# Kernel optimization log

Hardware: AMD Instinct MI355X
Metric: run time of the kernel (lower is better)

The kernel has to match this reference:

```python
import jax, jax.numpy as jnp
import numpy as np

B, N, D, C = 32, 6, 41, 64
FH, FW = 4, 6            # 150//32, 200//32
IN_CH = 768
NX, NY, NZ = 200, 200, 1 # from x/y/zbound
DX = np.array([0.5, 0.5, 20.0], np.float32)
BX = np.array([-49.75, -49.75, 0.0], np.float32)  # bound[0] + step/2


def _frustum():
    # (D, FH, FW, 3) pixel-coord + depth frustum, matching create_frustum
    ds = np.arange(4.0, 45.0, 1.0, dtype=np.float32)             # D = 41
    xs = np.linspace(0.0, 200.0 - 1.0, FW, dtype=np.float32)
    ys = np.linspace(0.0, 150.0 - 1.0, FH, dtype=np.float32)
    g = np.stack(np.broadcast_arrays(xs[None, None, :], ys[None, :, None], ds[:, None, None]), axis=-1)
    return jnp.asarray(g)


def setup_inputs() -> dict:
    key = jax.random.key(0)
    k1, k2, k3 = jax.random.split(key, 3)
    x = jax.random.normal(k1, (B, N, IN_CH, FH, FW), jnp.float32)
    # cam-to-ego base rotation (cam z -> ego x, cam x -> -ego y, cam y -> -ego z)
    R0 = np.array([[0., 0., 1.], [-1., 0., 0.], [0., -1., 0.]], np.float32)
    yaw = 2.0 * np.pi * np.arange(N) / N
    cz, sz = np.cos(yaw).astype(np.float32), np.sin(yaw).astype(np.float32)
    Rz = np.zeros((N, 3, 3), np.float32)
    Rz[:, 0, 0] = cz; Rz[:, 0, 1] = -sz; Rz[:, 1, 0] = sz; Rz[:, 1, 1] = cz; Rz[:, 2, 2] = 1.0
    rots = jnp.asarray(np.broadcast_to((Rz @ R0)[None], (B, N, 3, 3)))
    K = np.array([[100., 0., 100.], [0., 100., 75.], [0., 0., 1.]], np.float32)
    intrins = jnp.asarray(np.broadcast_to(K, (B, N, 3, 3)))
    trans = jax.random.uniform(k2, (B, N, 3), jnp.float32, -2.0, 2.0)
    conv_w = jax.random.normal(k3, (D + C, IN_CH), jnp.float32) * 0.02
    conv_b = jnp.zeros((D + C,), jnp.float32)
    return {"x": x, "rots": rots, "trans": trans, "intrins": intrins, "conv_w": conv_w, "conv_b": conv_b}


def reference(x, rots, trans, intrins, conv_w, conv_b):
    frustum = _frustum()                                        # (D,FH,FW,3)
    # --- get_geometry ---
    pts = jnp.concatenate([frustum[..., :2] * frustum[..., 2:3], frustum[..., 2:3]], -1)
    combine = rots @ jnp.linalg.inv(intrins)                    # (B,N,3,3)
    geom = jnp.einsum('bnij,dhwj->bndhwi', combine, pts) + trans[:, :, None, None, None, :]
    # --- get_cam_feats: 1x1 conv depthnet, softmax depth, outer product ---
    xf = x.reshape(B * N, IN_CH, FH, FW)
    y = jnp.einsum('oc,bchw->bohw', conv_w, xf) + conv_b[None, :, None, None]
    depth_logit = y[:, :D]                                      # (BN,D,FH,FW)
    depth = jax.nn.softmax(depth_logit, axis=1)
    feat = y[:, D:D + C]                                        # (BN,C,FH,FW)
    xv = (depth[:, None] * feat[:, :, None]).reshape(B, N, C, D, FH, FW).transpose(0, 1, 3, 4, 5, 2)
    # --- voxel_pooling: segment-sum over voxel rank, scatter to BEV ---
    xN = xv.reshape(-1, C)                                      # (Nprime, C)
    g = ((geom - (BX - DX / 2.0)) / DX).astype(jnp.int32).reshape(-1, 3)  # trunc like .long()
    Np = xN.shape[0]
    bix = jnp.repeat(jnp.arange(Np // (Np // B) * 0 + B), Np // B)        # batch index per point
    kept = ((g[:, 0] >= 0) & (g[:, 0] < NX) & (g[:, 1] >= 0) & (g[:, 1] < NY)
            & (g[:, 2] >= 0) & (g[:, 2] < NZ))
    idx = ((bix * NZ + g[:, 2]) * NX + g[:, 0]) * NY + g[:, 1]
    idx = jnp.where(kept, idx, 0)
    xm = jnp.where(kept[:, None], xN, 0.0)
    pooled = jax.ops.segment_sum(xm, idx, num_segments=B * NZ * NX * NY)  # (B*NZ*NX*NY, C)
    final = pooled.reshape(B, NZ, NX, NY, C).transpose(0, 1, 4, 2, 3).reshape(B, NZ * C, NX, NY)
    return (final, depth_logit)
```

## Files before the change

kernel.cpp:

```cpp
#include <hip/hip_runtime.h>
#include <hip/hip_bf16.h>

#define B_    32
#define N_    6
#define D_    41
#define C_    64
#define FH_   4
#define FW_   6
#define INCH  768
#define HW    24
#define O_    105
#define PBN   984
#define PPB   5904
#define NPTS  188928
#define FINAL_ELEMS 81920000


__global__ __launch_bounds__(256) void k_conv(
    const float* __restrict__ x, const float* __restrict__ w,
    const float* __restrict__ bias,
    float* __restrict__ depth_ws, float* __restrict__ feat_ws,
    float* __restrict__ dlogit)
{
    const int bn = blockIdx.x;
    const int t  = threadIdx.x;
    __shared__ float ylds[O_ * HW];
    __shared__ float smax[HW], srs[HW];

    const float* xb0 = x + (size_t)bn * (INCH * HW);
    for (int u2 = t; u2 < O_ * 6; u2 += 256) {
        int o  = u2 / 6;
        int hq = (u2 % 6) * 4;
        const float* wr = w + (size_t)o * INCH;
        const float* xb = xb0 + hq;
        float a0 = 0.f, a1 = 0.f, a2 = 0.f, a3 = 0.f;
        for (int c = 0; c < INCH; ++c) {
            float wv = wr[c];
            float4 xv = *(const float4*)(xb + c * HW);
            a0 = __fadd_rn(a0, __fmul_rn(wv, xv.x));
            a1 = __fadd_rn(a1, __fmul_rn(wv, xv.y));
            a2 = __fadd_rn(a2, __fmul_rn(wv, xv.z));
            a3 = __fadd_rn(a3, __fmul_rn(wv, xv.w));
        }
        float bo = bias[o];
        ylds[o * HW + hq + 0] = __fadd_rn(a0, bo);
        ylds[o * HW + hq + 1] = __fadd_rn(a1, bo);
        ylds[o * HW + hq + 2] = __fadd_rn(a2, bo);
        ylds[o * HW + hq + 3] = __fadd_rn(a3, bo);
    }
    __syncthreads();

    if (t < HW) {
        float mx = -1e30f;
        for (int d = 0; d < D_; d++) mx = fmaxf(mx, ylds[d * HW + t]);
        float s = 0.f;
        for (int d = 0; d < D_; d++) s = __fadd_rn(s, expf(__fsub_rn(ylds[d * HW + t], mx)));
        smax[t] = mx; srs[t] = s;
    }
    __syncthreads();

    for (int u = t; u < D_ * HW; u += 256) {
        float yv = ylds[u];
        int hw = u % HW;
        depth_ws[bn * PBN + u] = __fdiv_rn(expf(__fsub_rn(yv, smax[hw])), srs[hw]);
        dlogit[(size_t)bn * PBN + u] = yv;
    }
    for (int u = t; u < C_ * HW; u += 256)
        feat_ws[bn * (C_ * HW) + u] = ylds[D_ * HW + u];
}

__global__ __launch_bounds__(256) void k_geom(
    const float* __restrict__ m1, const float* __restrict__ trans,
    const float* __restrict__ m2, int* __restrict__ vox)
{
    const float* rots = (fabsf(m1[0]) > 50.0f) ? m2 : m1;
    const float* intr = (fabsf(m1[0]) > 50.0f) ? m1 : m2;

    int p = blockIdx.x * 256 + threadIdx.x;
    int b  = p / PPB;
    int pl = p % PPB;
    int n  = pl / PBN;
    int r  = pl % PBN;
    int d  = r / HW;
    int hw = r % HW;
    int h = hw / FW_, wp = hw % FW_;

    float dv = 4.0f + (float)d;
    float xi = (float)((double)wp * (199.0 / 5.0));
    float yi = (float)((double)h  * (149.0 / 3.0));
    float px = __fmul_rn(xi, dv), py = __fmul_rn(yi, dv), pz = dv;

    int bn = b * N_ + n;
    const float* K = intr + bn * 9;
    const float* R = rots + bn * 9;
    const float* T = trans + bn * 3;

    float a00 = K[0], a01 = K[1], a02 = K[2];
    float a11 = K[4], a12 = K[5];
    float a22 = K[8];

    float i00 = __fdiv_rn(1.0f, a00);
    float i11 = __fdiv_rn(1.0f, a11);
    float x0  = __fmul_rn(a01, i00);
    float i01 = __fmul_rn(-i11, x0);
    float i22 = __fdiv_rn(1.0f, a22);
    float y0  = __fmul_rn(a02, i00);
    y0 = __fadd_rn(y0, __fmul_rn(a12, i01));
    float y1  = __fmul_rn(a12, i11);
    float i02 = __fmul_rn(-i22, y0);
    float i12 = __fmul_rn(-i22, y1);
    float i10 = 0.f, i20 = 0.f, i21 = 0.f;

    float r00 = R[0], r01 = R[1], r02 = R[2];
    float r10 = R[3], r11 = R[4], r12 = R[5];
    float r20 = R[6], r21 = R[7], r22 = R[8];

#define MM(u0,u1,u2, v0,v1,v2) \
    __fmaf_rn(u2, v2, __fmaf_rn(u1, v1, __fmul_rn(u0, v0)))
    float c00 = MM(r00, r01, r02, i00, i10, i20);
    float c01 = MM(r00, r01, r02, i01, i11, i21);
    float c02 = MM(r00, r01, r02, i02, i12, i22);
    float c10 = MM(r10, r11, r12, i00, i10, i20);
    float c11 = MM(r10, r11, r12, i01, i11, i21);
    float c12 = MM(r10, r11, r12, i02, i12, i22);
    float c20 = MM(r20, r21, r22, i00, i10, i20);
    float c21 = MM(r20, r21, r22, i01, i11, i21);
    float c22 = MM(r20, r21, r22, i02, i12, i22);
#undef MM

#define DOT3(u0,v0,u1,v1,u2,v2) \
    __fadd_rn(__fadd_rn(__fmul_rn(u0,v0), __fmul_rn(u1,v1)), __fmul_rn(u2,v2))
    float gx = __fadd_rn(DOT3(c00,px, c01,py, c02,pz), T[0]);
    float gy = __fadd_rn(DOT3(c10,px, c11,py, c12,pz), T[1]);
    float gz = __fadd_rn(DOT3(c20,px, c21,py, c22,pz), T[2]);
#undef DOT3

    int ix = (int)__fmul_rn(__fadd_rn(gx, 50.0f), 2.0f);
    int iy = (int)__fmul_rn(__fadd_rn(gy, 50.0f), 2.0f);
    int iz = (int)__fdiv_rn(__fadd_rn(gz, 10.0f), 20.0f);
    bool kept = (ix >= 0) && (ix < 200) && (iy >= 0) && (iy < 200) && (iz == 0);
    vox[p] = kept ? (ix * 200 + iy) : -1;
}

__global__ __launch_bounds__(256) void k_splat(
    const float* __restrict__ depth, const float* __restrict__ feat,
    const int* __restrict__ vox, float* __restrict__ out)
{
    __shared__ float plane[10000];
    int bid = blockIdx.x;
    int b   = bid >> 8;
    int rem = bid & 255;
    int c   = rem >> 2;
    int q   = rem & 3;
    int t   = threadIdx.x;

    for (int i = t; i < 10000; i += 256) plane[i] = 0.f;
    __syncthreads();

    const int lo = q * 10000;
    const float* fb = feat + (size_t)(b * N_) * (C_ * HW) + c * HW;
    for (int i = t; i < PPB; i += 256) {
        int p = b * PPB + i;
        int rel = vox[p] - lo;
        if ((unsigned)rel < 10000u) {
            int n  = i / PBN;
            int hw = i % HW;
            atomicAdd(&plane[rel], depth[p] * fb[n * (C_ * HW) + hw]);
        }
    }
    __syncthreads();

    float4* ob = (float4*)(out + ((size_t)(b * C_ + c) * 40000) + lo);
    const float4* pl4 = (const float4*)plane;
    for (int i = t; i < 2500; i += 256) ob[i] = pl4[i];
}

extern "C" void kernel_launch(void* const* d_in, const int* in_sizes, int n_in,
                              void* d_out, int out_size, void* d_ws, size_t ws_size,
                              hipStream_t stream) {
    const float *x = nullptr, *m1 = nullptr, *m2 = nullptr, *trn = nullptr,
                *w = nullptr, *bias = nullptr;
    for (int i = 0; i < n_in; i++) {
        const float* p = (const float*)d_in[i];
        switch (in_sizes[i]) {
            case 3538944: x = p; break;
            case 1728:    if (!m1) m1 = p; else m2 = p; break;
            case 576:     trn = p; break;
            case 80640:   w = p; break;
            case 105:     bias = p; break;
            default: break;
        }
    }
    if (!x)    x    = (const float*)d_in[0];
    if (!m1)   m1   = (const float*)d_in[1];
    if (!trn)  trn  = (const float*)d_in[2];
    if (!m2)   m2   = (const float*)d_in[3];
    if (!w)    w    = (const float*)d_in[4];
    if (!bias) bias = (const float*)d_in[5];

    float* depth_ws = (float*)d_ws;
    float* feat_ws  = depth_ws + NPTS;
    int*   vox      = (int*)(feat_ws + 192 * C_ * HW);

    float* out    = (float*)d_out;
    float* dlogit = out + FINAL_ELEMS;

    k_conv <<<192,  256, 0, stream>>>(x, w, bias, depth_ws, feat_ws, dlogit);
    k_geom <<<738,  256, 0, stream>>>(m1, trn, m2, vox);
    k_splat<<<8192, 256, 0, stream>>>(depth_ws, feat_ws, vox, out);
}
```

Before: 537.8 us.

## Split conv into a 576-block kernel and a separate softmax kernel

The 1x1 conv is split out of the fused conv+softmax kernel. Each camera's 630 output work items are now spread over 3 blocks of 210 threads, so 576 blocks run instead of 192, and the raw logits go to a global workspace. A separate softmax kernel reads that workspace to write depth probabilities and logits, and the splat kernel reads feature channels straight from the workspace, which drops the separate feature copy. This is meant to fill more of the GPU's compute units during the conv, at the cost of one extra launch and a round trip of the logits through global memory.

New measurement: 520.1 us. 3.3% less time.

```diff
diff --git a/kernel.cpp b/kernel.cpp
--- a/kernel.cpp
+++ b/kernel.cpp
@@ -13,60 +13,66 @@
 #define PBN   984
 #define PPB   5904
 #define NPTS  188928
+#define YSTR  2520
 #define FINAL_ELEMS 81920000
 
 
-__global__ __launch_bounds__(256) void k_conv(
+__global__ __launch_bounds__(256) void k_conv_y(
     const float* __restrict__ x, const float* __restrict__ w,
-    const float* __restrict__ bias,
-    float* __restrict__ depth_ws, float* __restrict__ feat_ws,
-    float* __restrict__ dlogit)
+    const float* __restrict__ bias, float* __restrict__ y_ws)
+{
+    const int bid  = blockIdx.x;
+    const int bn   = bid / 3;
+    const int part = bid % 3;
+    const int t    = threadIdx.x;
+    if (t >= 210) return;
+    const int u2 = part * 210 + t;
+    const int o  = u2 / 6;
+    const int hq = (u2 % 6) * 4;
+
+    const float* wr = w + (size_t)o * INCH;
+    const float* xb = x + (size_t)bn * (INCH * HW) + hq;
+    float a0 = 0.f, a1 = 0.f, a2 = 0.f, a3 = 0.f;
+    for (int c = 0; c < INCH; ++c) {
+        float wv = wr[c];
+        float4 xv = *(const float4*)(xb + c * HW);
+        a0 = __fadd_rn(a0, __fmul_rn(wv, xv.x));
+        a1 = __fadd_rn(a1, __fmul_rn(wv, xv.y));
+        a2 = __fadd_rn(a2, __fmul_rn(wv, xv.z));
+        a3 = __fadd_rn(a3, __fmul_rn(wv, xv.w));
+    }
+    float bo = bias[o];
+    float* dst = y_ws + (size_t)bn * YSTR + o * HW + hq;
+    dst[0] = __fadd_rn(a0, bo);
+    dst[1] = __fadd_rn(a1, bo);
+    dst[2] = __fadd_rn(a2, bo);
+    dst[3] = __fadd_rn(a3, bo);
+}
+
+__global__ __launch_bounds__(256) void k_softmax(
+    const float* __restrict__ y_ws,
+    float* __restrict__ depth_ws, float* __restrict__ dlogit)
 {
     const int bn = blockIdx.x;
     const int t  = threadIdx.x;
-    __shared__ float ylds[O_ * HW];
     __shared__ float smax[HW], srs[HW];
-
-    const float* xb0 = x + (size_t)bn * (INCH * HW);
-    for (int u2 = t; u2 < O_ * 6; u2 += 256) {
-        int o  = u2 / 6;
-        int hq = (u2 % 6) * 4;
-        const float* wr = w + (size_t)o * INCH;
-        const float* xb = xb0 + hq;
-        float a0 = 0.f, a1 = 0.f, a2 = 0.f, a3 = 0.f;
-        for (int c = 0; c < INCH; ++c) {
-            float wv = wr[c];
-            float4 xv = *(const float4*)(xb + c * HW);
-            a0 = __fadd_rn(a0, __fmul_rn(wv, xv.x));
-            a1 = __fadd_rn(a1, __fmul_rn(wv, xv.y));
-            a2 = __fadd_rn(a2, __fmul_rn(wv, xv.z));
-            a3 = __fadd_rn(a3, __fmul_rn(wv, xv.w));
-        }
-        float bo = bias[o];
-        ylds[o * HW + hq + 0] = __fadd_rn(a0, bo);
-        ylds[o * HW + hq + 1] = __fadd_rn(a1, bo);
-        ylds[o * HW + hq + 2] = __fadd_rn(a2, bo);
-        ylds[o * HW + hq + 3] = __fadd_rn(a3, bo);
-    }
-    __syncthreads();
+    const float* yb = y_ws + (size_t)bn * YSTR;
 
     if (t < HW) {
         float mx = -1e30f;
-        for (int d = 0; d < D_; d++) mx = fmaxf(mx, ylds[d * HW + t]);
+        for (int d = 0; d < D_; d++) mx = fmaxf(mx, yb[d * HW + t]);
         float s = 0.f;
-        for (int d = 0; d < D_; d++) s = __fadd_rn(s, expf(__fsub_rn(ylds[d * HW + t], mx)));
+        for (int d = 0; d < D_; d++) s = __fadd_rn(s, expf(__fsub_rn(yb[d * HW + t], mx)));
         smax[t] = mx; srs[t] = s;
     }
     __syncthreads();
 
     for (int u = t; u < D_ * HW; u += 256) {
-        float yv = ylds[u];
+        float yv = yb[u];
         int hw = u % HW;
         depth_ws[bn * PBN + u] = __fdiv_rn(expf(__fsub_rn(yv, smax[hw])), srs[hw]);
         dlogit[(size_t)bn * PBN + u] = yv;
     }
-    for (int u = t; u < C_ * HW; u += 256)
-        feat_ws[bn * (C_ * HW) + u] = ylds[D_ * HW + u];
 }
 
 __global__ __launch_bounds__(256) void k_geom(
@@ -143,7 +149,7 @@
 }
 
 __global__ __launch_bounds__(256) void k_splat(
-    const float* __restrict__ depth, const float* __restrict__ feat,
+    const float* __restrict__ depth, const float* __restrict__ y_ws,
     const int* __restrict__ vox, float* __restrict__ out)
 {
     __shared__ float plane[10000];
@@ -158,14 +164,14 @@
     __syncthreads();
 
     const int lo = q * 10000;
-    const float* fb = feat + (size_t)(b * N_) * (C_ * HW) + c * HW;
+    const float* fb = y_ws + (size_t)(b * N_) * YSTR + (D_ + c) * HW;
     for (int i = t; i < PPB; i += 256) {
         int p = b * PPB + i;
         int rel = vox[p] - lo;
         if ((unsigned)rel < 10000u) {
             int n  = i / PBN;
             int hw = i % HW;
-            atomicAdd(&plane[rel], depth[p] * fb[n * (C_ * HW) + hw]);
+            atomicAdd(&plane[rel], depth[p] * fb[n * YSTR + hw]);
         }
     }
     __syncthreads();
@@ -198,14 +204,15 @@
     if (!w)    w    = (const float*)d_in[4];
     if (!bias) bias = (const float*)d_in[5];
 
-    float* depth_ws = (float*)d_ws;
-    float* feat_ws  = depth_ws + NPTS;
-    int*   vox      = (int*)(feat_ws + 192 * C_ * HW);
+    float* y_ws     = (float*)d_ws;
+    float* depth_ws = y_ws + 192 * YSTR;
+    int*   vox      = (int*)(depth_ws + NPTS);
 
     float* out    = (float*)d_out;
     float* dlogit = out + FINAL_ELEMS;
 
-    k_conv <<<192,  256, 0, stream>>>(x, w, bias, depth_ws, feat_ws, dlogit);
-    k_geom <<<738,  256, 0, stream>>>(m1, trn, m2, vox);
-    k_splat<<<8192, 256, 0, stream>>>(depth_ws, feat_ws, vox, out);
-}
+    k_conv_y <<<576,  256, 0, stream>>>(x, w, bias, y_ws);
+    k_softmax<<<192,  256, 0, stream>>>(y_ws, depth_ws, dlogit);
+    k_geom   <<<738,  256, 0, stream>>>(m1, trn, m2, vox);
+    k_splat  <<<8192, 256, 0, stream>>>(depth_ws, y_ws, vox, out);
+}
```

## Stage input tile in LDS and register-block conv over 3 outputs

Applied to the files above, without the earlier changes.

The 1x1 conv kernel now loads each camera's input slice into shared memory in two halves. Each thread computes 3 output channels by 4 pixels with float4 weight loads and fma, so every x value read is reused across three outputs instead of being refetched from global memory per output. This is meant to cut global load traffic and instruction count in the conv, which was the serial per-block dot-product bottleneck. Using fma instead of separate rounded mul and add changes rounding slightly, and the workspace buffers are reordered.

New measurement: 458.5 us. -14.7%, faster.

```diff
diff --git a/kernel.cpp b/kernel.cpp
--- a/kernel.cpp
+++ b/kernel.cpp
@@ -16,57 +16,101 @@
 #define FINAL_ELEMS 81920000
 
 
-__global__ __launch_bounds__(256) void k_conv(
+__global__ __launch_bounds__(256) void k_conv_fused(
     const float* __restrict__ x, const float* __restrict__ w,
     const float* __restrict__ bias,
-    float* __restrict__ depth_ws, float* __restrict__ feat_ws,
+    float* __restrict__ feat_ws, float* __restrict__ depth_ws,
     float* __restrict__ dlogit)
 {
+    __shared__ float xs[9216];
+    __shared__ float ys[O_ * HW];
+    __shared__ float smax[HW], srs[HW];
+
     const int bn = blockIdx.x;
     const int t  = threadIdx.x;
-    __shared__ float ylds[O_ * HW];
-    __shared__ float smax[HW], srs[HW];
-
-    const float* xb0 = x + (size_t)bn * (INCH * HW);
-    for (int u2 = t; u2 < O_ * 6; u2 += 256) {
-        int o  = u2 / 6;
-        int hq = (u2 % 6) * 4;
-        const float* wr = w + (size_t)o * INCH;
-        const float* xb = xb0 + hq;
-        float a0 = 0.f, a1 = 0.f, a2 = 0.f, a3 = 0.f;
-        for (int c = 0; c < INCH; ++c) {
-            float wv = wr[c];
-            float4 xv = *(const float4*)(xb + c * HW);
-            a0 = __fadd_rn(a0, __fmul_rn(wv, xv.x));
-            a1 = __fadd_rn(a1, __fmul_rn(wv, xv.y));
-            a2 = __fadd_rn(a2, __fmul_rn(wv, xv.z));
-            a3 = __fadd_rn(a3, __fmul_rn(wv, xv.w));
-        }
-        float bo = bias[o];
-        ylds[o * HW + hq + 0] = __fadd_rn(a0, bo);
-        ylds[o * HW + hq + 1] = __fadd_rn(a1, bo);
-        ylds[o * HW + hq + 2] = __fadd_rn(a2, bo);
-        ylds[o * HW + hq + 3] = __fadd_rn(a3, bo);
+    const int og = t / 6;
+    const int q6 = t % 6;
+
+    float a[3][4] = {{0.f,0.f,0.f,0.f},{0.f,0.f,0.f,0.f},{0.f,0.f,0.f,0.f}};
+    const int o0 = og * 3;
+    const float4* wr0 = (const float4*)(w + (size_t)(o0 + 0) * INCH);
+    const float4* wr1 = (const float4*)(w + (size_t)(o0 + 1) * INCH);
+    const float4* wr2 = (const float4*)(w + (size_t)(o0 + 2) * INCH);
+    float4* xs4 = (float4*)xs;
+
+    for (int half = 0; half < 2; ++half) {
+        if (half) __syncthreads();
+        const float4* xg = (const float4*)(x + (size_t)bn * (INCH * HW)) + half * 2304;
+        for (int i = t; i < 2304; i += 256) xs4[i] = xg[i];
+        __syncthreads();
+
+        if (t < 210) {
+            const int wb = half * 96;
+            for (int c4 = 0; c4 < 96; ++c4) {
+                float4 w0 = wr0[wb + c4];
+                float4 w1 = wr1[wb + c4];
+                float4 w2 = wr2[wb + c4];
+                int cb = c4 * 4;
+                float4 x0 = xs4[(cb + 0) * 6 + q6];
+                float4 x1 = xs4[(cb + 1) * 6 + q6];
+                float4 x2 = xs4[(cb + 2) * 6 + q6];
+                float4 x3 = xs4[(cb + 3) * 6 + q6];
+                a[0][0]=fmaf(w0.x,x0.x,a[0][0]); a[0][1]=fmaf(w0.x,x0.y,a[0][1]);
+                a[0][2]=fmaf(w0.x,x0.z,a[0][2]); a[0][3]=fmaf(w0.x,x0.w,a[0][3]);
+                a[1][0]=fmaf(w1.x,x0.x,a[1][0]); a[1][1]=fmaf(w1.x,x0.y,a[1][1]);
+                a[1][2]=fmaf(w1.x,x0.z,a[1][2]); a[1][3]=fmaf(w1.x,x0.w,a[1][3]);
+                a[2][0]=fmaf(w2.x,x0.x,a[2][0]); a[2][1]=fmaf(w2.x,x0.y,a[2][1]);
+                a[2][2]=fmaf(w2.x,x0.z,a[2][2]); a[2][3]=fmaf(w2.x,x0.w,a[2][3]);
+                a[0][0]=fmaf(w0.y,x1.x,a[0][0]); a[0][1]=fmaf(w0.y,x1.y,a[0][1]);
+                a[0][2]=fmaf(w0.y,x1.z,a[0][2]); a[0][3]=fmaf(w0.y,x1.w,a[0][3]);
+                a[1][0]=fmaf(w1.y,x1.x,a[1][0]); a[1][1]=fmaf(w1.y,x1.y,a[1][1]);
+                a[1][2]=fmaf(w1.y,x1.z,a[1][2]); a[1][3]=fmaf(w1.y,x1.w,a[1][3]);
+                a[2][0]=fmaf(w2.y,x1.x,a[2][0]); a[2][1]=fmaf(w2.y,x1.y,a[2][1]);
+                a[2][2]=fmaf(w2.y,x1.z,a[2][2]); a[2][3]=fmaf(w2.y,x1.w,a[2][3]);
+                a[0][0]=fmaf(w0.z,x2.x,a[0][0]); a[0][1]=fmaf(w0.z,x2.y,a[0][1]);
+                a[0][2]=fmaf(w0.z,x2.z,a[0][2]); a[0][3]=fmaf(w0.z,x2.w,a[0][3]);
+                a[1][0]=fmaf(w1.z,x2.x,a[1][0]); a[1][1]=fmaf(w1.z,x2.y,a[1][1]);
+                a[1][2]=fmaf(w1.z,x2.z,a[1][2]); a[1][3]=fmaf(w1.z,x2.w,a[1][3]);
+                a[2][0]=fmaf(w2.z,x2.x,a[2][0]); a[2][1]=fmaf(w2.z,x2.y,a[2][1]);
+                a[2][2]=fmaf(w2.z,x2.z,a[2][2]); a[2][3]=fmaf(w2.z,x2.w,a[2][3]);
+                a[0][0]=fmaf(w0.w,x3.x,a[0][0]); a[0][1]=fmaf(w0.w,x3.y,a[0][1]);
+                a[0][2]=fmaf(w0.w,x3.z,a[0][2]); a[0][3]=fmaf(w0.w,x3.w,a[0][3]);
+                a[1][0]=fmaf(w1.w,x3.x,a[1][0]); a[1][1]=fmaf(w1.w,x3.y,a[1][1]);
+                a[1][2]=fmaf(w1.w,x3.z,a[1][2]); a[1][3]=fmaf(w1.w,x3.w,a[1][3]);
+                a[2][0]=fmaf(w2.w,x3.x,a[2][0]); a[2][1]=fmaf(w2.w,x3.y,a[2][1]);
+                a[2][2]=fmaf(w2.w,x3.z,a[2][2]); a[2][3]=fmaf(w2.w,x3.w,a[2][3]);
+            }
+        }
+    }
+
+    if (t < 210) {
+#pragma unroll
+        for (int r = 0; r < 3; r++) {
+            float bo = bias[o0 + r];
+#pragma unroll
+            for (int j = 0; j < 4; j++)
+                ys[(o0 + r) * HW + q6 * 4 + j] = a[r][j] + bo;
+        }
     }
     __syncthreads();
 
     if (t < HW) {
         float mx = -1e30f;
-        for (int d = 0; d < D_; d++) mx = fmaxf(mx, ylds[d * HW + t]);
+        for (int d = 0; d < D_; d++) mx = fmaxf(mx, ys[d * HW + t]);
         float s = 0.f;
-        for (int d = 0; d < D_; d++) s = __fadd_rn(s, expf(__fsub_rn(ylds[d * HW + t], mx)));
+        for (int d = 0; d < D_; d++) s = __fadd_rn(s, expf(__fsub_rn(ys[d * HW + t], mx)));
         smax[t] = mx; srs[t] = s;
     }
     __syncthreads();
 
     for (int u = t; u < D_ * HW; u += 256) {
-        float yv = ylds[u];
+        float yv = ys[u];
         int hw = u % HW;
         depth_ws[bn * PBN + u] = __fdiv_rn(expf(__fsub_rn(yv, smax[hw])), srs[hw]);
         dlogit[(size_t)bn * PBN + u] = yv;
     }
     for (int u = t; u < C_ * HW; u += 256)
-        feat_ws[bn * (C_ * HW) + u] = ylds[D_ * HW + u];
+        feat_ws[(size_t)bn * (C_ * HW) + u] = ys[D_ * HW + u];
 }
 
 __global__ __launch_bounds__(256) void k_geom(
@@ -198,14 +242,14 @@
     if (!w)    w    = (const float*)d_in[4];
     if (!bias) bias = (const float*)d_in[5];
 
-    float* depth_ws = (float*)d_ws;
-    float* feat_ws  = depth_ws + NPTS;
-    int*   vox      = (int*)(feat_ws + 192 * C_ * HW);
+    float* feat_ws  = (float*)d_ws;
+    float* depth_ws = feat_ws + 192 * C_ * HW;
+    int*   vox      = (int*)(depth_ws + NPTS);
 
     float* out    = (float*)d_out;
     float* dlogit = out + FINAL_ELEMS;
 
-    k_conv <<<192,  256, 0, stream>>>(x, w, bias, depth_ws, feat_ws, dlogit);
-    k_geom <<<738,  256, 0, stream>>>(m1, trn, m2, vox);
-    k_splat<<<8192, 256, 0, stream>>>(depth_ws, feat_ws, vox, out);
-}
+    k_conv_fused<<<192,  256, 0, stream>>>(x, w, bias, feat_ws, depth_ws, dlogit);
+    k_geom      <<<738,  256, 0, stream>>>(m1, trn, m2, vox);
+    k_splat     <<<8192, 256, 0, stream>>>(depth_ws, feat_ws, vox, out);
+}
```
